# Kernel optimization log

Hardware: AMD Instinct MI355X
Metric: run time of the kernel (lower is better)

The kernel has to match this reference:

```python
import jax, jax.numpy as jnp
import numpy as np

B, N, C_Z, H, C_H, W = 1, 192, 128, 4, 32, 16


def _layer_norm(x, w, b, eps=1e-5):
    mu = jnp.mean(x, axis=-1, keepdims=True)
    var = jnp.mean(jnp.square(x - mu), axis=-1, keepdims=True)
    return (x - mu) * jax.lax.rsqrt(var + eps) * w + b


def setup_inputs() -> dict:
    key = jax.random.key(0)
    ks = jax.random.split(key, 10)
    s = 0.02
    return {
        "z": jax.random.normal(ks[0], (B, N, N, C_Z), jnp.float32),
        "mask": jnp.ones((B, N, N), jnp.float32),
        "ln_w": jnp.ones((C_Z,), jnp.float32),
        "ln_b": jnp.zeros((C_Z,), jnp.float32),
        "w_q": jax.random.normal(ks[1], (C_Z, H * C_H), jnp.float32) * s,
        "w_k": jax.random.normal(ks[2], (C_Z, H * C_H), jnp.float32) * s,
        "w_v": jax.random.normal(ks[3], (C_Z, H * C_H), jnp.float32) * s,
        "w_bias": jax.random.normal(ks[4], (C_Z, H), jnp.float32) * s,
        "w_gate": jax.random.normal(ks[5], (C_Z, H * C_H), jnp.float32) * s,
        "b_gate": jnp.ones((H * C_H,), jnp.float32),
        "w_out": jax.random.normal(ks[6], (H * C_H, C_Z), jnp.float32) * s,
        "b_out": jnp.zeros((C_Z,), jnp.float32),
        "window_size": W,
    }


def reference(z, mask, ln_w, ln_b, w_q, w_k, w_v, w_bias, w_gate, b_gate, w_out, b_out, window_size):
    b, n = z.shape[0], z.shape[1]
    h = w_bias.shape[1]
    c = w_q.shape[1] // h
    w = int(window_size)

    zl = _layer_norm(z, ln_w, ln_b)                       # [B,N,N,Cz]
    q = (zl @ w_q).reshape(b, n, n, h, c)                 # [B,I,J,H,c]
    k = (zl @ w_k).reshape(b, n, n, h, c)
    v = (zl @ w_v).reshape(b, n, n, h, c)
    tb = zl @ w_bias                                      # [B,J,K,H] triangle bias

    # sliding window indices along the key axis, centered at each query j
    idx = jnp.arange(n)[:, None] - (w // 2) + jnp.arange(w)[None, :]   # [N,W]
    valid = (idx >= 0) & (idx < n)                                     # [N,W]
    idx_c = jnp.clip(idx, 0, n - 1)

    k_win = k[:, :, idx_c]                                # [B,I,J,W,H,c]
    v_win = v[:, :, idx_c]                                # [B,I,J,W,H,c]
    tb_win = jnp.take_along_axis(tb, idx_c[None, :, :, None], axis=2)  # [B,J,W,H]
    mask_win = mask[:, :, idx_c] * valid[None, None].astype(mask.dtype)  # [B,I,J,W]

    scale = 1.0 / jnp.sqrt(jnp.asarray(c, z.dtype))
    logits = jnp.einsum('bijhc,bijwhc->bijwh', q * scale, k_win)       # [B,I,J,W,H]
    logits = logits + tb_win[:, None]                                  # bias b_{j,k} broadcast over i
    logits = logits + jnp.where(mask_win > 0, 0.0, -1e9)[..., None]
    attn = jax.nn.softmax(logits, axis=3)

    o = jnp.einsum('bijwh,bijwhc->bijhc', attn, v_win)                 # [B,I,J,H,c]
    g = jax.nn.sigmoid(zl @ w_gate + b_gate).reshape(b, n, n, h, c)
    o = (g * o).reshape(b, n, n, h * c)
    return o @ w_out + b_out                                           # [B,I,J,Cz]
```

## Files before the change

### kernel.cpp

```cpp
#include <hip/hip_runtime.h>
#include <hip/hip_bf16.h>

#define N 192
#define CZ 128
#define NH 4
#define CH 32
#define WIN 16
#define NROWS (N*N)
#define RPB 144

typedef __attribute__((ext_vector_type(8))) short bf16x8;
typedef __attribute__((ext_vector_type(4))) float f32x4;

static __device__ __forceinline__ ushort f2bf(float x){
    union{float f; unsigned u;} a; a.f = x;
    unsigned r = a.u + 0x7fffu + ((a.u>>16)&1u);
    return (ushort)(r>>16);
}
static __device__ __forceinline__ float bf2f(ushort s){
    union{unsigned u; float f;} a; a.u = ((unsigned)s)<<16;
    return a.f;
}

__global__ __launch_bounds__(256) void k_pack(
    const float* __restrict__ wq, const float* __restrict__ wk,
    const float* __restrict__ wv, const float* __restrict__ wg,
    const float* __restrict__ wo, ushort* __restrict__ WP)
{
    const int m = blockIdx.y;
    const float* W = (m==0)?wq:(m==1)?wk:(m==2)?wv:(m==3)?wg:wo;
    const int f = blockIdx.x*256 + threadIdx.x;
    const int nt = f >> 8, ks = (f >> 6) & 3, lane8 = f & 63;
    const int col = nt*16 + (lane8 & 15);
    const int r0  = ks*32 + (lane8 >> 4)*8;
    ushort tmp[8];
    #pragma unroll
    for (int i=0; i<8; i++) tmp[i] = f2bf(W[(size_t)(r0+i)*CZ + col]);
    *(uint4*)(WP + (size_t)m*16384 + (size_t)f*8) = *(uint4*)tmp;
}

__global__ __launch_bounds__(256, 4) void k_proj(
    const float* __restrict__ z, const float* __restrict__ lnw, const float* __restrict__ lnb,
    const float* __restrict__ wbias, const ushort* __restrict__ WP,
    const float* __restrict__ bg,
    ushort* __restrict__ q, ushort* __restrict__ k,
    ushort* __restrict__ v, ushort* __restrict__ g, float* __restrict__ tb)
{
    __shared__ ushort zlds[RPB][132];
    __shared__ ushort st[4][16][36];
    const int rbase = blockIdx.x * RPB;
    const int tid  = threadIdx.x;
    const int wid  = tid >> 6, lane = tid & 63;
    const int l16  = lane & 15, lk = lane >> 4;

    {
        const float* zr0 = z + (size_t)(rbase + wid*4 + lk)*CZ + l16*8;
        float4 a = ((const float4*)zr0)[0];
        float4 b = ((const float4*)zr0)[1];
        for (int it = 0; it < 9; ++it) {
            float4 na, nb;
            if (it < 8) {
                const float* zr = z + (size_t)(rbase + (it+1)*16 + wid*4 + lk)*CZ + l16*8;
                na = ((const float4*)zr)[0];
                nb = ((const float4*)zr)[1];
            }
            const int r = it*16 + wid*4 + lk;
            float s  = a.x+a.y+a.z+a.w + b.x+b.y+b.z+b.w;
            float s2 = a.x*a.x+a.y*a.y+a.z*a.z+a.w*a.w + b.x*b.x+b.y*b.y+b.z*b.z+b.w*b.w;
            #pragma unroll
            for (int off=1; off<16; off<<=1) { s += __shfl_xor(s, off); s2 += __shfl_xor(s2, off); }
            const float mu   = s * (1.f/CZ);
            const float rstd = rsqrtf(s2*(1.f/CZ) - mu*mu + 1e-5f);
            const int c0 = l16*8;
            float vals[8] = {a.x,a.y,a.z,a.w,b.x,b.y,b.z,b.w};
            float tbp[4] = {0.f,0.f,0.f,0.f};
            uint4 pk; ushort* ph = (ushort*)&pk;
            #pragma unroll
            for (int t=0; t<8; t++) {
                const float nv = (vals[t]-mu)*rstd*lnw[c0+t] + lnb[c0+t];
                ph[t] = f2bf(nv);
                float4 wb4 = *(const float4*)(wbias + (c0+t)*4);
                tbp[0] += nv*wb4.x; tbp[1] += nv*wb4.y;
                tbp[2] += nv*wb4.z; tbp[3] += nv*wb4.w;
            }
            *(uint4*)&zlds[r][c0] = pk;
            #pragma unroll
            for (int off=1; off<16; off<<=1) {
                #pragma unroll
                for (int h=0; h<4; h++) tbp[h] += __shfl_xor(tbp[h], off);
            }
            if (l16 == 0) *(float4*)(tb + (size_t)(rbase+r)*4) = make_float4(tbp[0],tbp[1],tbp[2],tbp[3]);
            a = na; b = nb;
        }
    }
    __syncthreads();

    for (int m = 0; m < 4; ++m) {
        const ushort* WPm = WP + (size_t)m*16384;
        ushort* O = (m==0)?q:(m==1)?k:(m==2)?v:g;

        bf16x8 bfrag[2][4];
        float4 bg4[2];
        #pragma unroll
        for (int nt2=0; nt2<2; nt2++) {
            const int nt = wid*2 + nt2;
            #pragma unroll
            for (int ks=0; ks<4; ks++)
                bfrag[nt2][ks] = *(const bf16x8*)(WPm + nt*2048 + ks*512 + lane*8);
            if (m == 3) bg4[nt2] = *(const float4*)(bg + wid*32 + nt2*16 + lk*4);
        }

        #pragma unroll 1
        for (int rt=0; rt<9; rt++) {
            bf16x8 af[4];
            #pragma unroll
            for (int ks=0; ks<4; ks++)
                af[ks] = *(const bf16x8*)&zlds[rt*16 + l16][ks*32 + lk*8];
            #pragma unroll
            for (int nt2=0; nt2<2; nt2++) {
                f32x4 acc = {0.f,0.f,0.f,0.f};
                #pragma unroll
                for (int ks=0; ks<4; ks++)
                    acc = __builtin_amdgcn_mfma_f32_16x16x32_bf16(bfrag[nt2][ks], af[ks], acc, 0, 0, 0);
                float v0,v1,v2,v3;
                if (m == 3) {
                    v0 = 1.f/(1.f + __expf(-(acc[0] + bg4[nt2].x)));
                    v1 = 1.f/(1.f + __expf(-(acc[1] + bg4[nt2].y)));
                    v2 = 1.f/(1.f + __expf(-(acc[2] + bg4[nt2].z)));
                    v3 = 1.f/(1.f + __expf(-(acc[3] + bg4[nt2].w)));
                } else { v0=acc[0]; v1=acc[1]; v2=acc[2]; v3=acc[3]; }
                uint2 pk2;
                pk2.x = (unsigned)f2bf(v0) | ((unsigned)f2bf(v1)<<16);
                pk2.y = (unsigned)f2bf(v2) | ((unsigned)f2bf(v3)<<16);
                *(uint2*)&st[wid][l16][nt2*16 + lk*4] = pk2;
            }
            const int row = lane >> 2, c8 = lane & 3;
            uint4 ov = *(const uint4*)&st[wid][row][c8*8];
            *(uint4*)(O + (size_t)(rbase + rt*16 + row)*CZ + wid*32 + c8*8) = ov;
        }
    }
}

__global__ __launch_bounds__(256, 4) void k_attn_out(
    const ushort* __restrict__ q, const ushort* __restrict__ k, const ushort* __restrict__ v,
    const ushort* __restrict__ g, const float* __restrict__ tb, const float* __restrict__ mask,
    const ushort* __restrict__ WPo, const float* __restrict__ bout, float* __restrict__ out)
{
    __shared__ ushort kl[47][NH][40];
    __shared__ ushort vl[47][NH][40];
    __shared__ float  ml[47];
    ushort (*po)[136] = (ushort (*)[136])&kl[0][0][0];

    const int i   = blockIdx.y;
    const int j0  = blockIdx.x * 32;
    const int tid = threadIdx.x;

    for (int idx = tid; idx < 47*16; idx += 256) {
        const int row = idx >> 4, c8 = idx & 15;
        const int jj  = j0 - 8 + row;
        const int jjc = min(max(jj, 0), N-1);
        const size_t goff = ((size_t)i*N + jjc)*CZ + c8*8;
        const int hh = c8 >> 2, co = (c8 & 3)*8;
        *(uint4*)&kl[row][hh][co] = *(const uint4*)(k + goff);
        *(uint4*)&vl[row][hh][co] = *(const uint4*)(v + goff);
    }
    if (tid < 47) {
        const int jj  = j0 - 8 + tid;
        const int jjc = min(max(jj, 0), N-1);
        const bool ok = (jj >= 0) && (jj < N) && (mask[(size_t)i*N + jjc] > 0.f);
        ml[tid] = ok ? 0.f : -1e9f;
    }
    __syncthreads();

    const int chalf = tid & 1;
    const int h     = (tid >> 1) & 3;
    const int jloc  = tid >> 3;
    const int j     = j0 + jloc;
    const int c0l   = chalf * 16;
    const size_t base = ((size_t)i*N + j)*CZ + h*CH + c0l;

    float qv[16];
    {
        uint4 q1 = *(const uint4*)(q + base);
        uint4 q2 = *(const uint4*)(q + base + 8);
        const ushort* s1 = (const ushort*)&q1;
        const ushort* s2 = (const ushort*)&q2;
        #pragma unroll
        for (int t=0; t<8; t++) { qv[t] = bf2f(s1[t]); qv[8+t] = bf2f(s2[t]); }
    }

    const float scale = 0.17677669529663688f;
    float lg[WIN];
    #pragma unroll
    for (int w=0; w<WIN; w++) {
        const int rel = jloc + w;
        float dot = 0.f;
        #pragma unroll
        for (int c4=0; c4<2; c4++) {
            uint4 kv = *(const uint4*)&kl[rel][h][c0l + c4*8];
            const ushort* kp = (const ushort*)&kv;
            #pragma unroll
            for (int t=0; t<8; t++) dot += qv[c4*8+t]*bf2f(kp[t]);
        }
        dot += __shfl_xor(dot, 1);
        const int jj  = j - 8 + w;
        const int jjc = min(max(jj, 0), N-1);
        lg[w] = dot*scale + tb[((size_t)j*N + jjc)*4 + h] + ml[rel];
    }
    float mx = lg[0];
    #pragma unroll
    for (int w=1; w<WIN; w++) mx = fmaxf(mx, lg[w]);
    float sum = 0.f;
    #pragma unroll
    for (int w=0; w<WIN; w++) { lg[w] = __expf(lg[w]-mx); sum += lg[w]; }
    const float inv = 1.f/sum;

    float o[16];
    #pragma unroll
    for (int c=0; c<16; c++) o[c] = 0.f;
    #pragma unroll
    for (int w=0; w<WIN; w++) {
        const float p   = lg[w]*inv;
        const int   rel = jloc + w;
        #pragma unroll
        for (int c4=0; c4<2; c4++) {
            uint4 vv = *(const uint4*)&vl[rel][h][c0l + c4*8];
            const ushort* vp = (const ushort*)&vv;
            #pragma unroll
            for (int t=0; t<8; t++) o[c4*8+t] += p*bf2f(vp[t]);
        }
    }

    uint4 o1, o2;
    {
        uint4 g1 = *(const uint4*)(g + base);
        uint4 g2 = *(const uint4*)(g + base + 8);
        const ushort* s1 = (const ushort*)&g1;
        const ushort* s2 = (const ushort*)&g2;
        ushort* p1 = (ushort*)&o1; ushort* p2 = (ushort*)&o2;
        #pragma unroll
        for (int t=0; t<8; t++) {
            p1[t] = f2bf(o[t]   * bf2f(s1[t]));
            p2[t] = f2bf(o[8+t] * bf2f(s2[t]));
        }
    }
    __syncthreads();
    *(uint4*)&po[jloc][h*CH + c0l]     = o1;
    *(uint4*)&po[jloc][h*CH + c0l + 8] = o2;

    const int wid = tid >> 6, lane = tid & 63;
    const int l16 = lane & 15, lk = lane >> 4;
    bf16x8 bfrag[2][4];
    float4 bo4[2];
    #pragma unroll
    for (int nt2=0; nt2<2; nt2++) {
        const int nt = wid*2 + nt2;
        #pragma unroll
        for (int ks=0; ks<4; ks++)
            bfrag[nt2][ks] = *(const bf16x8*)(WPo + nt*2048 + ks*512 + lane*8);
        bo4[nt2] = *(const float4*)(bout + wid*32 + nt2*16 + lk*4);
    }
    __syncthreads();

    #pragma unroll
    for (int rt=0; rt<2; rt++) {
        bf16x8 af[4];
        #pragma unroll
        for (int ks=0; ks<4; ks++)
            af[ks] = *(const bf16x8*)&po[rt*16 + l16][ks*32 + lk*8];
        const size_t orow = (size_t)(i*N + j0 + rt*16 + l16)*CZ;
        #pragma unroll
        for (int nt2=0; nt2<2; nt2++) {
            f32x4 acc = {0.f,0.f,0.f,0.f};
            #pragma unroll
            for (int ks=0; ks<4; ks++)
                acc = __builtin_amdgcn_mfma_f32_16x16x32_bf16(bfrag[nt2][ks], af[ks], acc, 0, 0, 0);
            float4 ov;
            ov.x = acc[0] + bo4[nt2].x; ov.y = acc[1] + bo4[nt2].y;
            ov.z = acc[2] + bo4[nt2].z; ov.w = acc[3] + bo4[nt2].w;
            *(float4*)(out + orow + wid*32 + nt2*16 + lk*4) = ov;
        }
    }
}

extern "C" void kernel_launch(void* const* d_in, const int* in_sizes, int n_in,
                              void* d_out, int out_size, void* d_ws, size_t ws_size,
                              hipStream_t stream)
{
    const float* z    = (const float*)d_in[0];
    const float* mask = (const float*)d_in[1];
    const float* lnw  = (const float*)d_in[2];
    const float* lnb  = (const float*)d_in[3];
    const float* wq   = (const float*)d_in[4];
    const float* wk   = (const float*)d_in[5];
    const float* wv   = (const float*)d_in[6];
    const float* wb   = (const float*)d_in[7];
    const float* wg   = (const float*)d_in[8];
    const float* bg   = (const float*)d_in[9];
    const float* wo   = (const float*)d_in[10];
    const float* bo   = (const float*)d_in[11];

    const size_t NE = (size_t)NROWS*CZ;
    ushort* q  = (ushort*)d_ws;
    ushort* k  = q + NE;
    ushort* v  = k + NE;
    ushort* g  = v + NE;
    float*  tb = (float*)(g + NE);
    ushort* WP = (ushort*)(tb + (size_t)NROWS*4);
    if (ws_size < 4*NE*sizeof(ushort) + (size_t)NROWS*4*sizeof(float) + 5*16384*sizeof(ushort)) return;

    k_pack<<<dim3(8,5), 256, 0, stream>>>(wq, wk, wv, wg, wo, WP);
    k_proj<<<NROWS/RPB, 256, 0, stream>>>(z, lnw, lnb, wb, WP, bg, q, k, v, g, tb);
    k_attn_out<<<dim3(N/32, N), 256, 0, stream>>>(q, k, v, g, tb, mask, WP + 4*16384, bo, (float*)d_out);
}
```

Measured before the change: 56.36 us.

## Fuse layernorm and QKVG projections into the attention kernel

Removes the separate projection kernel that wrote q, k, v and g to global memory in bf16. The attention blocks now layer-norm their own window of z rows, including halo rows, and compute K/V for 48 rows and Q/G for 32 rows with MFMA straight into shared memory. The triangle bias is split into a small separate kernel because it needs values across rows. In exchange, K/V are recomputed for halo rows (48 instead of 32 per block, about 1.5x), z is re-read with overlap, and the larger shared-memory footprint lowers occupancy.

```diff
diff --git a/kernel.cpp b/kernel.cpp
--- a/kernel.cpp
+++ b/kernel.cpp
@@ -7,7 +7,6 @@
 #define CH 32
 #define WIN 16
 #define NROWS (N*N)
-#define RPB 144
 
 typedef __attribute__((ext_vector_type(8))) short bf16x8;
 typedef __attribute__((ext_vector_type(4))) float f32x4;
@@ -39,136 +38,161 @@
     *(uint4*)(WP + (size_t)m*16384 + (size_t)f*8) = *(uint4*)tmp;
 }
 
-__global__ __launch_bounds__(256, 4) void k_proj(
+__global__ __launch_bounds__(256) void k_tb(
     const float* __restrict__ z, const float* __restrict__ lnw, const float* __restrict__ lnb,
-    const float* __restrict__ wbias, const ushort* __restrict__ WP,
-    const float* __restrict__ bg,
-    ushort* __restrict__ q, ushort* __restrict__ k,
-    ushort* __restrict__ v, ushort* __restrict__ g, float* __restrict__ tb)
+    const float* __restrict__ wbias, float* __restrict__ tb)
 {
-    __shared__ ushort zlds[RPB][132];
-    __shared__ ushort st[4][16][36];
-    const int rbase = blockIdx.x * RPB;
-    const int tid  = threadIdx.x;
-    const int wid  = tid >> 6, lane = tid & 63;
-    const int l16  = lane & 15, lk = lane >> 4;
-
-    {
-        const float* zr0 = z + (size_t)(rbase + wid*4 + lk)*CZ + l16*8;
-        float4 a = ((const float4*)zr0)[0];
-        float4 b = ((const float4*)zr0)[1];
-        for (int it = 0; it < 9; ++it) {
-            float4 na, nb;
-            if (it < 8) {
-                const float* zr = z + (size_t)(rbase + (it+1)*16 + wid*4 + lk)*CZ + l16*8;
-                na = ((const float4*)zr)[0];
-                nb = ((const float4*)zr)[1];
-            }
-            const int r = it*16 + wid*4 + lk;
-            float s  = a.x+a.y+a.z+a.w + b.x+b.y+b.z+b.w;
-            float s2 = a.x*a.x+a.y*a.y+a.z*a.z+a.w*a.w + b.x*b.x+b.y*b.y+b.z*b.z+b.w*b.w;
-            #pragma unroll
-            for (int off=1; off<16; off<<=1) { s += __shfl_xor(s, off); s2 += __shfl_xor(s2, off); }
-            const float mu   = s * (1.f/CZ);
-            const float rstd = rsqrtf(s2*(1.f/CZ) - mu*mu + 1e-5f);
-            const int c0 = l16*8;
-            float vals[8] = {a.x,a.y,a.z,a.w,b.x,b.y,b.z,b.w};
-            float tbp[4] = {0.f,0.f,0.f,0.f};
-            uint4 pk; ushort* ph = (ushort*)&pk;
-            #pragma unroll
-            for (int t=0; t<8; t++) {
-                const float nv = (vals[t]-mu)*rstd*lnw[c0+t] + lnb[c0+t];
-                ph[t] = f2bf(nv);
-                float4 wb4 = *(const float4*)(wbias + (c0+t)*4);
-                tbp[0] += nv*wb4.x; tbp[1] += nv*wb4.y;
-                tbp[2] += nv*wb4.z; tbp[3] += nv*wb4.w;
-            }
-            *(uint4*)&zlds[r][c0] = pk;
-            #pragma unroll
-            for (int off=1; off<16; off<<=1) {
-                #pragma unroll
-                for (int h=0; h<4; h++) tbp[h] += __shfl_xor(tbp[h], off);
-            }
-            if (l16 == 0) *(float4*)(tb + (size_t)(rbase+r)*4) = make_float4(tbp[0],tbp[1],tbp[2],tbp[3]);
-            a = na; b = nb;
-        }
+    const int tid = threadIdx.x;
+    const int wave = tid >> 6, lane = tid & 63;
+    const int r  = wave*4 + (lane >> 4);
+    const int li = lane & 15;
+    const int row = blockIdx.x*16 + r;
+    const float* zr = z + (size_t)row*CZ + li*8;
+    float4 a = ((const float4*)zr)[0];
+    float4 b = ((const float4*)zr)[1];
+    float s  = a.x+a.y+a.z+a.w + b.x+b.y+b.z+b.w;
+    float s2 = a.x*a.x+a.y*a.y+a.z*a.z+a.w*a.w + b.x*b.x+b.y*b.y+b.z*b.z+b.w*b.w;
+    #pragma unroll
+    for (int off=1; off<16; off<<=1) { s += __shfl_xor(s, off); s2 += __shfl_xor(s2, off); }
+    const float mu   = s * (1.f/CZ);
+    const float rstd = rsqrtf(s2*(1.f/CZ) - mu*mu + 1e-5f);
+    const int c0 = li*8;
+    float vals[8] = {a.x,a.y,a.z,a.w,b.x,b.y,b.z,b.w};
+    float tbp[4] = {0.f,0.f,0.f,0.f};
+    #pragma unroll
+    for (int t=0; t<8; t++) {
+        const float nv = (vals[t]-mu)*rstd*lnw[c0+t] + lnb[c0+t];
+        float4 wb4 = *(const float4*)(wbias + (c0+t)*4);
+        tbp[0] += nv*wb4.x; tbp[1] += nv*wb4.y;
+        tbp[2] += nv*wb4.z; tbp[3] += nv*wb4.w;
+    }
+    #pragma unroll
+    for (int off=1; off<16; off<<=1) {
+        #pragma unroll
+        for (int h=0; h<4; h++) tbp[h] += __shfl_xor(tbp[h], off);
+    }
+    if (li == 0) *(float4*)(tb + (size_t)row*4) = make_float4(tbp[0],tbp[1],tbp[2],tbp[3]);
+}
+
+__global__ __launch_bounds__(256, 2) void k_fused(
+    const float* __restrict__ z, const float* __restrict__ lnw, const float* __restrict__ lnb,
+    const float* __restrict__ mask, const float* __restrict__ tb,
+    const ushort* __restrict__ WP, const float* __restrict__ bg,
+    const float* __restrict__ bout, float* __restrict__ out)
+{
+    __shared__ ushort zlds[48][132];
+    __shared__ ushort kl[48][NH][40];
+    __shared__ ushort vl[48][NH][40];
+    __shared__ ushort qb[32][136];
+    __shared__ ushort gb[32][136];
+    __shared__ float  ml[48];
+    ushort (*po)[136] = (ushort (*)[136])&zlds[0][0];
+
+    const int i   = blockIdx.y;
+    const int j0  = blockIdx.x * 32;
+    const int tid = threadIdx.x;
+    const int wid = tid >> 6, lane = tid & 63;
+    const int l16 = lane & 15, lk = lane >> 4;
+
+    for (int it = 0; it < 3; ++it) {
+        const int r   = it*16 + wid*4 + lk;
+        const int jj  = j0 - 8 + r;
+        const int jjc = min(max(jj, 0), N-1);
+        const float* zr = z + ((size_t)i*N + jjc)*CZ + l16*8;
+        float4 a = ((const float4*)zr)[0];
+        float4 b = ((const float4*)zr)[1];
+        float s  = a.x+a.y+a.z+a.w + b.x+b.y+b.z+b.w;
+        float s2 = a.x*a.x+a.y*a.y+a.z*a.z+a.w*a.w + b.x*b.x+b.y*b.y+b.z*b.z+b.w*b.w;
+        #pragma unroll
+        for (int off=1; off<16; off<<=1) { s += __shfl_xor(s, off); s2 += __shfl_xor(s2, off); }
+        const float mu   = s * (1.f/CZ);
+        const float rstd = rsqrtf(s2*(1.f/CZ) - mu*mu + 1e-5f);
+        const int c0 = l16*8;
+        float vals[8] = {a.x,a.y,a.z,a.w,b.x,b.y,b.z,b.w};
+        uint4 pk; ushort* ph = (ushort*)&pk;
+        #pragma unroll
+        for (int t=0; t<8; t++)
+            ph[t] = f2bf((vals[t]-mu)*rstd*lnw[c0+t] + lnb[c0+t]);
+        *(uint4*)&zlds[r][c0] = pk;
+    }
+    if (tid < 47) {
+        const int jj  = j0 - 8 + tid;
+        const int jjc = min(max(jj, 0), N-1);
+        const bool ok = (jj >= 0) && (jj < N) && (mask[(size_t)i*N + jjc] > 0.f);
+        ml[tid] = ok ? 0.f : -1e9f;
     }
     __syncthreads();
 
-    for (int m = 0; m < 4; ++m) {
-        const ushort* WPm = WP + (size_t)m*16384;
-        ushort* O = (m==0)?q:(m==1)?k:(m==2)?v:g;
-
+    #pragma unroll 1
+    for (int m = 1; m <= 2; ++m) {
         bf16x8 bfrag[2][4];
-        float4 bg4[2];
-        #pragma unroll
-        for (int nt2=0; nt2<2; nt2++) {
-            const int nt = wid*2 + nt2;
+        #pragma unroll
+        for (int nt2=0; nt2<2; nt2++)
             #pragma unroll
             for (int ks=0; ks<4; ks++)
-                bfrag[nt2][ks] = *(const bf16x8*)(WPm + nt*2048 + ks*512 + lane*8);
-            if (m == 3) bg4[nt2] = *(const float4*)(bg + wid*32 + nt2*16 + lk*4);
-        }
-
-        #pragma unroll 1
-        for (int rt=0; rt<9; rt++) {
+                bfrag[nt2][ks] = *(const bf16x8*)(WP + (size_t)m*16384 + (wid*2+nt2)*2048 + ks*512 + lane*8);
+        ushort (*dst)[NH][40] = (m==1) ? kl : vl;
+        #pragma unroll
+        for (int t=0; t<3; ++t) {
+            const int slot0 = t*16;
             bf16x8 af[4];
             #pragma unroll
             for (int ks=0; ks<4; ks++)
-                af[ks] = *(const bf16x8*)&zlds[rt*16 + l16][ks*32 + lk*8];
+                af[ks] = *(const bf16x8*)&zlds[slot0 + l16][ks*32 + lk*8];
             #pragma unroll
             for (int nt2=0; nt2<2; nt2++) {
                 f32x4 acc = {0.f,0.f,0.f,0.f};
                 #pragma unroll
                 for (int ks=0; ks<4; ks++)
                     acc = __builtin_amdgcn_mfma_f32_16x16x32_bf16(bfrag[nt2][ks], af[ks], acc, 0, 0, 0);
-                float v0,v1,v2,v3;
-                if (m == 3) {
-                    v0 = 1.f/(1.f + __expf(-(acc[0] + bg4[nt2].x)));
-                    v1 = 1.f/(1.f + __expf(-(acc[1] + bg4[nt2].y)));
-                    v2 = 1.f/(1.f + __expf(-(acc[2] + bg4[nt2].z)));
-                    v3 = 1.f/(1.f + __expf(-(acc[3] + bg4[nt2].w)));
-                } else { v0=acc[0]; v1=acc[1]; v2=acc[2]; v3=acc[3]; }
                 uint2 pk2;
-                pk2.x = (unsigned)f2bf(v0) | ((unsigned)f2bf(v1)<<16);
-                pk2.y = (unsigned)f2bf(v2) | ((unsigned)f2bf(v3)<<16);
-                *(uint2*)&st[wid][l16][nt2*16 + lk*4] = pk2;
+                pk2.x = (unsigned)f2bf(acc[0]) | ((unsigned)f2bf(acc[1])<<16);
+                pk2.y = (unsigned)f2bf(acc[2]) | ((unsigned)f2bf(acc[3])<<16);
+                *(uint2*)&dst[slot0 + l16][wid][nt2*16 + lk*4] = pk2;
             }
-            const int row = lane >> 2, c8 = lane & 3;
-            uint4 ov = *(const uint4*)&st[wid][row][c8*8];
-            *(uint4*)(O + (size_t)(rbase + rt*16 + row)*CZ + wid*32 + c8*8) = ov;
-        }
-    }
-}
-
-__global__ __launch_bounds__(256, 4) void k_attn_out(
-    const ushort* __restrict__ q, const ushort* __restrict__ k, const ushort* __restrict__ v,
-    const ushort* __restrict__ g, const float* __restrict__ tb, const float* __restrict__ mask,
-    const ushort* __restrict__ WPo, const float* __restrict__ bout, float* __restrict__ out)
-{
-    __shared__ ushort kl[47][NH][40];
-    __shared__ ushort vl[47][NH][40];
-    __shared__ float  ml[47];
-    ushort (*po)[136] = (ushort (*)[136])&kl[0][0][0];
-
-    const int i   = blockIdx.y;
-    const int j0  = blockIdx.x * 32;
-    const int tid = threadIdx.x;
-
-    for (int idx = tid; idx < 47*16; idx += 256) {
-        const int row = idx >> 4, c8 = idx & 15;
-        const int jj  = j0 - 8 + row;
-        const int jjc = min(max(jj, 0), N-1);
-        const size_t goff = ((size_t)i*N + jjc)*CZ + c8*8;
-        const int hh = c8 >> 2, co = (c8 & 3)*8;
-        *(uint4*)&kl[row][hh][co] = *(const uint4*)(k + goff);
-        *(uint4*)&vl[row][hh][co] = *(const uint4*)(v + goff);
-    }
-    if (tid < 47) {
-        const int jj  = j0 - 8 + tid;
-        const int jjc = min(max(jj, 0), N-1);
-        const bool ok = (jj >= 0) && (jj < N) && (mask[(size_t)i*N + jjc] > 0.f);
-        ml[tid] = ok ? 0.f : -1e9f;
+        }
+    }
+    {
+        #pragma unroll 1
+        for (int mm = 0; mm < 2; ++mm) {
+            const int m = mm ? 3 : 0;
+            bf16x8 bfrag[2][4];
+            float4 bg4[2];
+            #pragma unroll
+            for (int nt2=0; nt2<2; nt2++) {
+                #pragma unroll
+                for (int ks=0; ks<4; ks++)
+                    bfrag[nt2][ks] = *(const bf16x8*)(WP + (size_t)m*16384 + (wid*2+nt2)*2048 + ks*512 + lane*8);
+                if (mm) bg4[nt2] = *(const float4*)(bg + wid*32 + nt2*16 + lk*4);
+            }
+            #pragma unroll
+            for (int t=0; t<2; ++t) {
+                const int slot0 = 8 + t*16;
+                bf16x8 af[4];
+                #pragma unroll
+                for (int ks=0; ks<4; ks++)
+                    af[ks] = *(const bf16x8*)&zlds[slot0 + l16][ks*32 + lk*8];
+                #pragma unroll
+                for (int nt2=0; nt2<2; nt2++) {
+                    f32x4 acc = {0.f,0.f,0.f,0.f};
+                    #pragma unroll
+                    for (int ks=0; ks<4; ks++)
+                        acc = __builtin_amdgcn_mfma_f32_16x16x32_bf16(bfrag[nt2][ks], af[ks], acc, 0, 0, 0);
+                    float v0,v1,v2,v3;
+                    if (mm) {
+                        v0 = 1.f/(1.f + __expf(-(acc[0] + bg4[nt2].x)));
+                        v1 = 1.f/(1.f + __expf(-(acc[1] + bg4[nt2].y)));
+                        v2 = 1.f/(1.f + __expf(-(acc[2] + bg4[nt2].z)));
+                        v3 = 1.f/(1.f + __expf(-(acc[3] + bg4[nt2].w)));
+                    } else { v0=acc[0]; v1=acc[1]; v2=acc[2]; v3=acc[3]; }
+                    uint2 pk2;
+                    pk2.x = (unsigned)f2bf(v0) | ((unsigned)f2bf(v1)<<16);
+                    pk2.y = (unsigned)f2bf(v2) | ((unsigned)f2bf(v3)<<16);
+                    if (mm) *(uint2*)&gb[t*16 + l16][wid*32 + nt2*16 + lk*4] = pk2;
+                    else    *(uint2*)&qb[t*16 + l16][wid*32 + nt2*16 + lk*4] = pk2;
+                }
+            }
+        }
     }
     __syncthreads();
 
@@ -177,12 +201,11 @@
     const int jloc  = tid >> 3;
     const int j     = j0 + jloc;
     const int c0l   = chalf * 16;
-    const size_t base = ((size_t)i*N + j)*CZ + h*CH + c0l;
 
     float qv[16];
     {
-        uint4 q1 = *(const uint4*)(q + base);
-        uint4 q2 = *(const uint4*)(q + base + 8);
+        uint4 q1 = *(const uint4*)&qb[jloc][h*CH + c0l];
+        uint4 q2 = *(const uint4*)&qb[jloc][h*CH + c0l + 8];
         const ushort* s1 = (const ushort*)&q1;
         const ushort* s2 = (const ushort*)&q2;
         #pragma unroll
@@ -233,8 +256,8 @@
 
     uint4 o1, o2;
     {
-        uint4 g1 = *(const uint4*)(g + base);
-        uint4 g2 = *(const uint4*)(g + base + 8);
+        uint4 g1 = *(const uint4*)&gb[jloc][h*CH + c0l];
+        uint4 g2 = *(const uint4*)&gb[jloc][h*CH + c0l + 8];
         const ushort* s1 = (const ushort*)&g1;
         const ushort* s2 = (const ushort*)&g2;
         ushort* p1 = (ushort*)&o1; ushort* p2 = (ushort*)&o2;
@@ -244,20 +267,16 @@
             p2[t] = f2bf(o[8+t] * bf2f(s2[t]));
         }
     }
-    __syncthreads();
     *(uint4*)&po[jloc][h*CH + c0l]     = o1;
     *(uint4*)&po[jloc][h*CH + c0l + 8] = o2;
 
-    const int wid = tid >> 6, lane = tid & 63;
-    const int l16 = lane & 15, lk = lane >> 4;
     bf16x8 bfrag[2][4];
     float4 bo4[2];
     #pragma unroll
     for (int nt2=0; nt2<2; nt2++) {
-        const int nt = wid*2 + nt2;
         #pragma unroll
         for (int ks=0; ks<4; ks++)
-            bfrag[nt2][ks] = *(const bf16x8*)(WPo + nt*2048 + ks*512 + lane*8);
+            bfrag[nt2][ks] = *(const bf16x8*)(WP + (size_t)4*16384 + (wid*2+nt2)*2048 + ks*512 + lane*8);
         bo4[nt2] = *(const float4*)(bout + wid*32 + nt2*16 + lk*4);
     }
     __syncthreads();
@@ -300,16 +319,11 @@
     const float* wo   = (const float*)d_in[10];
     const float* bo   = (const float*)d_in[11];
 
-    const size_t NE = (size_t)NROWS*CZ;
-    ushort* q  = (ushort*)d_ws;
-    ushort* k  = q + NE;
-    ushort* v  = k + NE;
-    ushort* g  = v + NE;
-    float*  tb = (float*)(g + NE);
+    float*  tb = (float*)d_ws;
     ushort* WP = (ushort*)(tb + (size_t)NROWS*4);
-    if (ws_size < 4*NE*sizeof(ushort) + (size_t)NROWS*4*sizeof(float) + 5*16384*sizeof(ushort)) return;
-
-    k_pack<<<dim3(8,5), 256, 0, stream>>>(wq, wk, wv, wg, wo, WP);
-    k_proj<<<NROWS/RPB, 256, 0, stream>>>(z, lnw, lnb, wb, WP, bg, q, k, v, g, tb);
-    k_attn_out<<<dim3(N/32, N), 256, 0, stream>>>(q, k, v, g, tb, mask, WP + 4*16384, bo, (float*)d_out);
-}
+    if (ws_size < (size_t)NROWS*4*sizeof(float) + 5*16384*sizeof(ushort)) return;
+
+    k_pack <<<dim3(8,5), 256, 0, stream>>>(wq, wk, wv, wg, wo, WP);
+    k_tb   <<<NROWS/16, 256, 0, stream>>>(z, lnw, lnb, wb, tb);
+    k_fused<<<dim3(N/32, N), 256, 0, stream>>>(z, lnw, lnb, mask, tb, WP, bg, bo, (float*)d_out);
+}
```

New measurement: 56.29 us. Within noise of the previous version (-0.1%).
